# Kernel optimization log

Measured on AMD Instinct MI355X. Metric: run time of the kernel, lower is better.

The kernel has to match this reference:

```python
import jax, jax.numpy as jnp
import numpy as np


def setup_inputs() -> dict:
    key = jax.random.key(0)
    inp = jax.random.normal(key, (32, 1024, 1024), dtype=jnp.float32)
    return {"inp": inp}


def reference(inp):
    n = inp.shape[0]  # static trip count, matches inp.size(0)

    def body(i, a):
        b = a * 2.0
        b = a + b            # b = 3*a
        s = jnp.sum(b)
        # predicated branch: a += b if s > 0 else a -= b
        return jnp.where(s > 0.0, a + b, a - b)

    return jax.lax.fori_loop(0, n, body, inp)
```

## Files before the change

kernel.cpp:

```cpp
#include <hip/hip_runtime.h>


#define RGRID 2048

__global__ __launch_bounds__(256) void reduce_sum_kernel(
        const float4* __restrict__ in, float* __restrict__ partials, int n4) {
    int tid    = blockIdx.x * blockDim.x + threadIdx.x;
    int stride = gridDim.x * blockDim.x;
    float s = 0.0f;
    for (int i = tid; i < n4; i += stride) {
        float4 v = in[i];
        s += (v.x + v.y) + (v.z + v.w);
    }
    #pragma unroll
    for (int off = 32; off > 0; off >>= 1)
        s += __shfl_down(s, off, 64);
    __shared__ float lds[4];
    int lane = threadIdx.x & 63;
    int wid  = threadIdx.x >> 6;
    if (lane == 0) lds[wid] = s;
    __syncthreads();
    if (threadIdx.x == 0) {
        partials[blockIdx.x] = (lds[0] + lds[1]) + (lds[2] + lds[3]);
    }
}

__global__ __launch_bounds__(256) void scale_kernel(
        const float4* __restrict__ in, float4* __restrict__ out,
        const float* __restrict__ partials, int n4) {
    int lane = threadIdx.x & 63;
    float s = 0.0f;
    #pragma unroll
    for (int j = 0; j < RGRID / 64; ++j)
        s += partials[j * 64 + lane];
    #pragma unroll
    for (int off = 32; off > 0; off >>= 1)
        s += __shfl_down(s, off, 64);
    float S = __shfl(s, 0, 64);

    float m = (S > 0.0f) ? 0x1p64f : ((S < 0.0f) ? -0x1p63f : 0x1p32f);
    int tid    = blockIdx.x * blockDim.x + threadIdx.x;
    int stride = gridDim.x * blockDim.x;
    for (int i = tid; i < n4; i += stride) {
        float4 v = in[i];
        v.x *= m; v.y *= m; v.z *= m; v.w *= m;
        out[i] = v;
    }
}

extern "C" void kernel_launch(void* const* d_in, const int* in_sizes, int n_in,
                              void* d_out, int out_size, void* d_ws, size_t ws_size,
                              hipStream_t stream) {
    const float* in = (const float*)d_in[0];
    float* out      = (float*)d_out;
    float* ws       = (float*)d_ws;
    int n  = in_sizes[0];
    int n4 = n >> 2;

    const int BLK = 256;
    reduce_sum_kernel<<<RGRID, BLK, 0, stream>>>((const float4*)in, ws, n4);
    scale_kernel<<<RGRID, BLK, 0, stream>>>((const float4*)in, (float4*)out, ws, n4);
}
```

Measured before the change: 245.2 us.

## Fuse reduction with speculative positive-sum scaling and add conditional fixup pass

The reduction kernel now also writes the output, betting that the global sum is positive and scaling by the corresponding constant. A second kernel combines the partial sums and returns immediately when the bet holds. Otherwise it rescales the output in place by a correction factor. This removes one full read of the input when the sum is positive, but adds an extra read and write pass over the output when it is not.

New measurement: 231.8 us. -5.5%, faster.

```diff
diff --git a/kernel.cpp b/kernel.cpp
--- a/kernel.cpp
+++ b/kernel.cpp
@@ -2,15 +2,21 @@
 
 
 #define RGRID 2048
+#define BLK   256
 
-__global__ __launch_bounds__(256) void reduce_sum_kernel(
-        const float4* __restrict__ in, float* __restrict__ partials, int n4) {
+__global__ __launch_bounds__(256) void fused_reduce_scale_kernel(
+        const float4* __restrict__ in, float4* __restrict__ out,
+        float* __restrict__ partials, int n4) {
     int tid    = blockIdx.x * blockDim.x + threadIdx.x;
     int stride = gridDim.x * blockDim.x;
+    const float m = 0x1p64f;
     float s = 0.0f;
     for (int i = tid; i < n4; i += stride) {
         float4 v = in[i];
         s += (v.x + v.y) + (v.z + v.w);
+        float4 w;
+        w.x = v.x * m; w.y = v.y * m; w.z = v.z * m; w.w = v.w * m;
+        out[i] = w;
     }
     #pragma unroll
     for (int off = 32; off > 0; off >>= 1)
@@ -20,14 +26,12 @@
     int wid  = threadIdx.x >> 6;
     if (lane == 0) lds[wid] = s;
     __syncthreads();
-    if (threadIdx.x == 0) {
+    if (threadIdx.x == 0)
         partials[blockIdx.x] = (lds[0] + lds[1]) + (lds[2] + lds[3]);
-    }
 }
 
-__global__ __launch_bounds__(256) void scale_kernel(
-        const float4* __restrict__ in, float4* __restrict__ out,
-        const float* __restrict__ partials, int n4) {
+__global__ __launch_bounds__(256) void fixup_kernel(
+        float4* __restrict__ out, const float* __restrict__ partials, int n4) {
     int lane = threadIdx.x & 63;
     float s = 0.0f;
     #pragma unroll
@@ -38,12 +42,14 @@
         s += __shfl_down(s, off, 64);
     float S = __shfl(s, 0, 64);
 
-    float m = (S > 0.0f) ? 0x1p64f : ((S < 0.0f) ? -0x1p63f : 0x1p32f);
+    float f = (S > 0.0f) ? 1.0f : ((S < 0.0f) ? -0x1p-1f : 0x1p-32f);
+    if (f == 1.0f) return;
+
     int tid    = blockIdx.x * blockDim.x + threadIdx.x;
     int stride = gridDim.x * blockDim.x;
     for (int i = tid; i < n4; i += stride) {
-        float4 v = in[i];
-        v.x *= m; v.y *= m; v.z *= m; v.w *= m;
+        float4 v = out[i];
+        v.x *= f; v.y *= f; v.z *= f; v.w *= f;
         out[i] = v;
     }
 }
@@ -57,7 +63,8 @@
     int n  = in_sizes[0];
     int n4 = n >> 2;
 
-    const int BLK = 256;
-    reduce_sum_kernel<<<RGRID, BLK, 0, stream>>>((const float4*)in, ws, n4);
-    scale_kernel<<<RGRID, BLK, 0, stream>>>((const float4*)in, (float4*)out, ws, n4);
+    fused_reduce_scale_kernel<<<RGRID, BLK, 0, stream>>>(
+        (const float4*)in, (float4*)out, ws, n4);
+    fixup_kernel<<<RGRID, BLK, 0, stream>>>(
+        (float4*)out, ws, n4);
 }
```
